# Kernel tuning notes

Measured on AMD Instinct MI355X. Metric: run time of the kernel, lower is better.

The kernel has to match this reference:

```python
import jax, jax.numpy as jnp
import numpy as np

N = 16384
S = 7
B = 2
C = 20
LAMBD_COORD = 5.0
LAMBD_NOOBJ = 0.5
EPS = 1e-6


def _rel2abs(box):
    """Convert (xcr_rcell, ycr_rcell, wr, hr, ...) cell-relative boxes on an
    (N,S,S,>=4) grid to absolute corner boxes (xmin,ymin,xmax,ymax) in [0,1]."""
    col = jnp.arange(S, dtype=box.dtype)[None, None, :]  # x cell index j
    row = jnp.arange(S, dtype=box.dtype)[None, :, None]  # y cell index i
    xc = (box[..., 0] + col) / S
    yc = (box[..., 1] + row) / S
    w = box[..., 2]
    h = box[..., 3]
    half_w = w * 0.5
    half_h = h * 0.5
    return jnp.stack([xc - half_w, yc - half_h, xc + half_w, yc + half_h], axis=-1)


def _iou(b1, b2):
    """Elementwise IoU of corner boxes (..., 4)."""
    xi1 = jnp.maximum(b1[..., 0], b2[..., 0])
    yi1 = jnp.maximum(b1[..., 1], b2[..., 1])
    xi2 = jnp.minimum(b1[..., 2], b2[..., 2])
    yi2 = jnp.minimum(b1[..., 3], b2[..., 3])
    inter = jnp.clip(xi2 - xi1, 0.0) * jnp.clip(yi2 - yi1, 0.0)
    a1 = (b1[..., 2] - b1[..., 0]) * (b1[..., 3] - b1[..., 1])
    a2 = (b2[..., 2] - b2[..., 0]) * (b2[..., 3] - b2[..., 1])
    return inter / (a1 + a2 - inter + EPS)


def setup_inputs() -> dict:
    key = jax.random.key(0)
    k1, k2, k3, k4 = jax.random.split(key, 4)
    prediction = jax.random.uniform(k1, (N, S, S, B * 5 + C), dtype=jnp.float32)
    conf = (jax.random.uniform(k2, (N, S, S)) > 0.7).astype(jnp.float32)[..., None]
    boxes = jax.random.uniform(k3, (N, S, S, 4), dtype=jnp.float32) * conf
    cls = jax.nn.one_hot(jax.random.randint(k4, (N, S, S), 0, C), C, dtype=jnp.float32) * conf
    target = jnp.concatenate([boxes, conf, cls], axis=-1)  # (N,S,S,5+C)
    return {"prediction": prediction, "target": target}


def reference(prediction, target):
    n = prediction.shape[0]

    # Absolute boxes; target box zeroed where no object (mul by confidence).
    tgt_abs = _rel2abs(target[..., :5]) * target[..., 4:5]
    pred_abs1 = _rel2abs(prediction[..., :5])
    pred_abs2 = _rel2abs(prediction[..., 5:10])

    iou1 = _iou(tgt_abs, pred_abs1)  # (N,S,S)
    iou2 = _iou(tgt_abs, pred_abs2)

    # Faithful to torch: idx = (iou1 > iou2)*5, i.e. gather box2 when iou1 > iou2.
    pick_box2 = (iou1 > iou2)[..., None]
    xywhc_hat = jnp.where(pick_box2, prediction[..., 5:10], prediction[..., :5])

    xy_hat = xywhc_hat[..., :2]
    wh_hat = xywhc_hat[..., 2:4]
    c_hat = xywhc_hat[..., 4:5]

    xy = target[..., :2]
    wh = target[..., 2:4]
    conf = target[..., 4:5]
    noobj = conf == 0.0  # identity_obj in torch code

    def sse(t, p):
        return jnp.sum((t - p) ** 2)

    # _coordloss: clamp(min=0), zero where noobj, sum-MSE / N
    loss_xy = sse(xy, jnp.where(noobj, 0.0, jnp.clip(xy_hat, 0.0))) / n
    # _sizeloss: clamp(min=0), zero where noobj, sqrt(sum + eps) / N
    loss_wh = jnp.sqrt(sse(wh, jnp.where(noobj, 0.0, jnp.clip(wh_hat, 0.0))) + EPS) / n
    # _confidenceloss: clamp to [0,1], mask, sum-MSE / N (obj and noobj variants)
    c_hat_clamped = jnp.clip(c_hat, 0.0, 1.0)
    loss_conf_obj = sse(conf, jnp.where(noobj, 0.0, c_hat_clamped)) / n
    loss_conf_noobj = sse(conf, jnp.where(~noobj, 0.0, c_hat_clamped)) / n
    # _classloss: no clamp, zero where noobj
    loss_class = sse(target[..., 5:], jnp.where(noobj, 0.0, prediction[..., 10:])) / n

    loss = (LAMBD_COORD * loss_xy + LAMBD_COORD * loss_wh + loss_conf_obj
            + LAMBD_NOOBJ * loss_conf_noobj + loss_class)
    return (loss_xy, loss_wh, loss_conf_obj, loss_conf_noobj, loss_class, loss)
```

## Files before the change

kernel.cpp:

```cpp
#include <hip/hip_runtime.h>
#include <math.h>

constexpr int TOT    = 16384 * 7 * 7;
constexpr int TILE   = 64;
constexpr int NTILES = TOT / TILE;
constexpr int NBLK   = 1280;
constexpr int NSLOT  = 64;
constexpr int SLOT_STRIDE = 32;
constexpr float INV_N = 1.0f / 16384.0f;
constexpr float INV7  = 1.0f / 7.0f;

constexpr int PRED_TILE_B = TILE * 30 * 4;
constexpr int TGT_TILE_B  = TILE * 25 * 4;
constexpr int BUF_B       = 14336;

__device__ __forceinline__ float fast_rcp(float x) {
    return __builtin_amdgcn_rcpf(x);
}

__device__ __forceinline__ void dma16(const void* g, void* lds) {
    __builtin_amdgcn_global_load_lds(
        (const __attribute__((address_space(1))) void*)g,
        (__attribute__((address_space(3))) void*)lds, 16, 0, 0);
}

__global__ __launch_bounds__(64) void yolo_partial(
    const float* __restrict__ pred, const float* __restrict__ tgt,
    float* __restrict__ acc )
{
    __shared__ float4 smem4[2 * BUF_B / 16];
    char* smem = (char*)smem4;

    const int l   = threadIdx.x;
    const int bid = blockIdx.x;

    float a_xy = 0.0f, a_wh = 0.0f, a_co = 0.0f, a_cn = 0.0f, a_cl = 0.0f;

    const int nt = (NTILES - bid + NBLK - 1) / NBLK;

    auto stage = [&](int tile, int b) {
        const char* gp = (const char*)pred + (long)tile * PRED_TILE_B;
        const char* gt = (const char*)tgt  + (long)tile * TGT_TILE_B;
        char* lb = smem + b * BUF_B;
#pragma unroll
        for (int i = 0; i < 7; ++i)
            dma16(gp + (size_t)(l + i * 64) * 16, lb + i * 1024);
        if (l < 32) dma16(gp + (size_t)(l + 448) * 16, lb + 7168);
#pragma unroll
        for (int i = 0; i < 6; ++i)
            dma16(gt + (size_t)(l + i * 64) * 16, lb + 7680 + i * 1024);
        if (l < 16) dma16(gt + (size_t)(l + 384) * 16, lb + 13824);
    };

    stage(bid, 0);
    int buf = 0;

    for (int k = 0; k < nt; ++k) {
        const int tile = bid + k * NBLK;
        if (k + 1 < nt) {
            stage(bid + (k + 1) * NBLK, buf ^ 1);
            asm volatile("s_waitcnt vmcnt(15)" ::: "memory");
        } else {
            asm volatile("s_waitcnt vmcnt(0)" ::: "memory");
        }
        __builtin_amdgcn_sched_barrier(0);

        const float* pred_s = (const float*)(smem + buf * BUF_B);
        const float* tgt_s  = pred_s + TILE * 30;

        const int   cell = tile * TILE + l;
        const int   col  = cell % 7;
        const int   row  = (cell / 7) % 7;
        const float fcol = (float)col, frow = (float)row;

        float pv[30];
        {
            const float2* p2 = reinterpret_cast<const float2*>(pred_s + l * 30);
#pragma unroll
            for (int i = 0; i < 15; ++i) {
                float2 v = p2[i];
                pv[2 * i] = v.x; pv[2 * i + 1] = v.y;
            }
        }
        float tv[25];
        {
            const float* tp = tgt_s + l * 25;
#pragma unroll
            for (int kk = 0; kk < 25; ++kk) tv[kk] = tp[kk];
        }

        const float conf  = tv[4];
        const bool  noobj = (conf == 0.0f);

        float xc = (tv[0] + fcol) * INV7, yc = (tv[1] + frow) * INV7;
        float hw = tv[2] * 0.5f,          hh = tv[3] * 0.5f;
        float tx1 = (xc - hw) * conf, ty1 = (yc - hh) * conf;
        float tx2 = (xc + hw) * conf, ty2 = (yc + hh) * conf;
        float t_area = (tx2 - tx1) * (ty2 - ty1);

        float xc1 = (pv[0] + fcol) * INV7, yc1 = (pv[1] + frow) * INV7;
        float hw1 = pv[2] * 0.5f,          hh1 = pv[3] * 0.5f;
        float bx1 = xc1 - hw1, by1 = yc1 - hh1, bx2 = xc1 + hw1, by2 = yc1 + hh1;
        float xi1 = fmaxf(tx1, bx1), yi1 = fmaxf(ty1, by1);
        float xi2 = fminf(tx2, bx2), yi2 = fminf(ty2, by2);
        float inter1 = fmaxf(xi2 - xi1, 0.0f) * fmaxf(yi2 - yi1, 0.0f);
        float area1  = (bx2 - bx1) * (by2 - by1);
        float iou1 = inter1 * fast_rcp(t_area + area1 - inter1 + 1e-6f);

        float xc2 = (pv[5] + fcol) * INV7, yc2 = (pv[6] + frow) * INV7;
        float hw2 = pv[7] * 0.5f,          hh2 = pv[8] * 0.5f;
        float cx1 = xc2 - hw2, cy1 = yc2 - hh2, cx2 = xc2 + hw2, cy2 = yc2 + hh2;
        float xj1 = fmaxf(tx1, cx1), yj1 = fmaxf(ty1, cy1);
        float xj2 = fminf(tx2, cx2), yj2 = fminf(ty2, cy2);
        float inter2 = fmaxf(xj2 - xj1, 0.0f) * fmaxf(yj2 - yj1, 0.0f);
        float area2  = (cx2 - cx1) * (cy2 - cy1);
        float iou2 = inter2 * fast_rcp(t_area + area2 - inter2 + 1e-6f);

        const bool pick2 = iou1 > iou2;
        float hx  = pick2 ? pv[5] : pv[0];
        float hy  = pick2 ? pv[6] : pv[1];
        float hwv = pick2 ? pv[7] : pv[2];
        float hhv = pick2 ? pv[8] : pv[3];
        float hc  = pick2 ? pv[9] : pv[4];

        float px = noobj ? 0.0f : fmaxf(hx, 0.0f);
        float py = noobj ? 0.0f : fmaxf(hy, 0.0f);
        float dx = tv[0] - px, dy = tv[1] - py;
        a_xy += dx * dx + dy * dy;
        float pw = noobj ? 0.0f : fmaxf(hwv, 0.0f);
        float ph = noobj ? 0.0f : fmaxf(hhv, 0.0f);
        float dw = tv[2] - pw, dh = tv[3] - ph;
        a_wh += dw * dw + dh * dh;
        float cc = fminf(fmaxf(hc, 0.0f), 1.0f);
        float co = noobj ? 0.0f : cc;
        float cn = noobj ? cc : 0.0f;
        float dco = conf - co, dcn = conf - cn;
        a_co += dco * dco;
        a_cn += dcn * dcn;
        float cl = 0.0f;
#pragma unroll
        for (int kk = 0; kk < 20; ++kk) {
            float pc = noobj ? 0.0f : pv[10 + kk];
            float d  = tv[5 + kk] - pc;
            cl += d * d;
        }
        a_cl += cl;

        buf ^= 1;
    }

#pragma unroll
    for (int off = 32; off > 0; off >>= 1) {
        a_xy += __shfl_down(a_xy, off);
        a_wh += __shfl_down(a_wh, off);
        a_co += __shfl_down(a_co, off);
        a_cn += __shfl_down(a_cn, off);
        a_cl += __shfl_down(a_cl, off);
    }
    if (l == 0) {
        float* slot = acc + (bid & (NSLOT - 1)) * SLOT_STRIDE;
        atomicAdd(&slot[0], a_xy);
        atomicAdd(&slot[1], a_wh);
        atomicAdd(&slot[2], a_co);
        atomicAdd(&slot[3], a_cn);
        atomicAdd(&slot[4], a_cl);
    }
}

__global__ __launch_bounds__(64) void yolo_final(
    const float* __restrict__ acc, float* __restrict__ out)
{
    const int l = threadIdx.x;
    float s0 = acc[l * SLOT_STRIDE + 0];
    float s1 = acc[l * SLOT_STRIDE + 1];
    float s2 = acc[l * SLOT_STRIDE + 2];
    float s3 = acc[l * SLOT_STRIDE + 3];
    float s4 = acc[l * SLOT_STRIDE + 4];
#pragma unroll
    for (int off = 32; off > 0; off >>= 1) {
        s0 += __shfl_down(s0, off);
        s1 += __shfl_down(s1, off);
        s2 += __shfl_down(s2, off);
        s3 += __shfl_down(s3, off);
        s4 += __shfl_down(s4, off);
    }
    if (l == 0) {
        float lxy = s0 * INV_N;
        float lwh = sqrtf(s1 + 1e-6f) * INV_N;
        float lco = s2 * INV_N;
        float lcn = s3 * INV_N;
        float lcl = s4 * INV_N;
        out[0] = lxy;
        out[1] = lwh;
        out[2] = lco;
        out[3] = lcn;
        out[4] = lcl;
        out[5] = 5.0f * lxy + 5.0f * lwh + lco + 0.5f * lcn + lcl;
    }
}

extern "C" void kernel_launch(void* const* d_in, const int* in_sizes, int n_in,
                              void* d_out, int out_size, void* d_ws, size_t ws_size,
                              hipStream_t stream)
{
    const float* pred = (const float*)d_in[0];
    const float* tgt  = (const float*)d_in[1];
    float* out = (float*)d_out;
    float* acc = (float*)d_ws;

    hipMemsetAsync(acc, 0, NSLOT * SLOT_STRIDE * sizeof(float), stream);
    yolo_partial<<<NBLK, 64, 0, stream>>>(pred, tgt, acc);
    yolo_final<<<1, 64, 0, stream>>>(acc, out);
}
```

Measured before the change: 38.18 us.

## Load target tiles via registers and replace atomics with per-block partials

Measured after the change: 34.02 us (median of 2 runs). 1.12x faster.

```diff
diff --git a/kernel.cpp b/kernel.cpp
--- a/kernel.cpp
+++ b/kernel.cpp
@@ -5,8 +5,6 @@
 constexpr int TILE   = 64;
 constexpr int NTILES = TOT / TILE;
 constexpr int NBLK   = 1280;
-constexpr int NSLOT  = 64;
-constexpr int SLOT_STRIDE = 32;
 constexpr float INV_N = 1.0f / 16384.0f;
 constexpr float INV7  = 1.0f / 7.0f;
 
@@ -26,7 +24,7 @@
 
 __global__ __launch_bounds__(64) void yolo_partial(
     const float* __restrict__ pred, const float* __restrict__ tgt,
-    float* __restrict__ acc )
+    float* __restrict__ part )
 {
     __shared__ float4 smem4[2 * BUF_B / 16];
     char* smem = (char*)smem4;
@@ -38,27 +36,47 @@
 
     const int nt = (NTILES - bid + NBLK - 1) / NBLK;
 
-    auto stage = [&](int tile, int b) {
-        const char* gp = (const char*)pred + (long)tile * PRED_TILE_B;
-        const char* gt = (const char*)tgt  + (long)tile * TGT_TILE_B;
-        char* lb = smem + b * BUF_B;
-#pragma unroll
-        for (int i = 0; i < 7; ++i)
-            dma16(gp + (size_t)(l + i * 64) * 16, lb + i * 1024);
-        if (l < 32) dma16(gp + (size_t)(l + 448) * 16, lb + 7168);
-#pragma unroll
-        for (int i = 0; i < 6; ++i)
-            dma16(gt + (size_t)(l + i * 64) * 16, lb + 7680 + i * 1024);
-        if (l < 16) dma16(gt + (size_t)(l + 384) * 16, lb + 13824);
-    };
-
-    stage(bid, 0);
+    float4 tr0, tr1, tr2, tr3, tr4, tr5, tr6;
+
+#define LD_TGT(tile_)                                                       \
+    {                                                                       \
+        const float4* gt4 = reinterpret_cast<const float4*>(               \
+            tgt + (long)(tile_) * (TILE * 25));                             \
+        tr0 = gt4[l];        tr1 = gt4[l + 64];  tr2 = gt4[l + 128];        \
+        tr3 = gt4[l + 192];  tr4 = gt4[l + 256]; tr5 = gt4[l + 320];        \
+        if (l < 16) tr6 = gt4[l + 384];                                     \
+    }
+
+#define DMA_PRED(tile_, b)                                                  \
+    {                                                                       \
+        const char* gp = (const char*)pred + (long)(tile_) * PRED_TILE_B;   \
+        char* lb = smem + (b) * BUF_B;                                      \
+        _Pragma("unroll")                                                   \
+        for (int i = 0; i < 7; ++i)                                         \
+            dma16(gp + (size_t)(l + i * 64) * 16, lb + i * 1024);           \
+        if (l < 32) dma16(gp + (size_t)(l + 448) * 16, lb + 7168);          \
+    }
+
+#define ST_TGT(b)                                                           \
+    {                                                                       \
+        float4* st4 = reinterpret_cast<float4*>(smem + (b) * BUF_B + 7680); \
+        st4[l]       = tr0;  st4[l + 64]  = tr1;  st4[l + 128] = tr2;       \
+        st4[l + 192] = tr3;  st4[l + 256] = tr4;  st4[l + 320] = tr5;       \
+        if (l < 16) st4[l + 384] = tr6;                                     \
+    }
+
+    LD_TGT(bid);
+    DMA_PRED(bid, 0);
+    asm volatile("s_waitcnt vmcnt(8)" ::: "memory");
+    __builtin_amdgcn_sched_barrier(0);
+    ST_TGT(0);
     int buf = 0;
 
     for (int k = 0; k < nt; ++k) {
         const int tile = bid + k * NBLK;
         if (k + 1 < nt) {
-            stage(bid + (k + 1) * NBLK, buf ^ 1);
+            LD_TGT(bid + (k + 1) * NBLK);
+            DMA_PRED(bid + (k + 1) * NBLK, buf ^ 1);
             asm volatile("s_waitcnt vmcnt(15)" ::: "memory");
         } else {
             asm volatile("s_waitcnt vmcnt(0)" ::: "memory");
@@ -137,15 +155,21 @@
         float dco = conf - co, dcn = conf - cn;
         a_co += dco * dco;
         a_cn += dcn * dcn;
-        float cl = 0.0f;
+        float clv = 0.0f;
 #pragma unroll
         for (int kk = 0; kk < 20; ++kk) {
             float pc = noobj ? 0.0f : pv[10 + kk];
             float d  = tv[5 + kk] - pc;
-            cl += d * d;
-        }
-        a_cl += cl;
-
+            clv += d * d;
+        }
+        a_cl += clv;
+
+        if (k + 1 < nt) {
+            asm volatile("s_waitcnt vmcnt(8)" ::: "memory");
+            __builtin_amdgcn_sched_barrier(0);
+            ST_TGT(buf ^ 1);
+            __builtin_amdgcn_sched_barrier(0);
+        }
         buf ^= 1;
     }
 
@@ -158,24 +182,26 @@
         a_cl += __shfl_down(a_cl, off);
     }
     if (l == 0) {
-        float* slot = acc + (bid & (NSLOT - 1)) * SLOT_STRIDE;
-        atomicAdd(&slot[0], a_xy);
-        atomicAdd(&slot[1], a_wh);
-        atomicAdd(&slot[2], a_co);
-        atomicAdd(&slot[3], a_cn);
-        atomicAdd(&slot[4], a_cl);
-    }
-}
-
-__global__ __launch_bounds__(64) void yolo_final(
-    const float* __restrict__ acc, float* __restrict__ out)
+        float4* r = reinterpret_cast<float4*>(part + bid * 8);
+        r[0] = make_float4(a_xy, a_wh, a_co, a_cn);
+        r[1] = make_float4(a_cl, 0.0f, 0.0f, 0.0f);
+    }
+#undef LD_TGT
+#undef DMA_PRED
+#undef ST_TGT
+}
+
+__global__ __launch_bounds__(256) void yolo_final(
+    const float* __restrict__ part, float* __restrict__ out)
 {
-    const int l = threadIdx.x;
-    float s0 = acc[l * SLOT_STRIDE + 0];
-    float s1 = acc[l * SLOT_STRIDE + 1];
-    float s2 = acc[l * SLOT_STRIDE + 2];
-    float s3 = acc[l * SLOT_STRIDE + 3];
-    float s4 = acc[l * SLOT_STRIDE + 4];
+    const int t = threadIdx.x;
+    float s0 = 0.0f, s1 = 0.0f, s2 = 0.0f, s3 = 0.0f, s4 = 0.0f;
+#pragma unroll
+    for (int i = 0; i < NBLK / 256; ++i) {
+        const float4* r = reinterpret_cast<const float4*>(part + (t + i * 256) * 8);
+        float4 v0 = r[0], v1 = r[1];
+        s0 += v0.x; s1 += v0.y; s2 += v0.z; s3 += v0.w; s4 += v1.x;
+    }
 #pragma unroll
     for (int off = 32; off > 0; off >>= 1) {
         s0 += __shfl_down(s0, off);
@@ -184,12 +210,24 @@
         s3 += __shfl_down(s3, off);
         s4 += __shfl_down(s4, off);
     }
-    if (l == 0) {
-        float lxy = s0 * INV_N;
-        float lwh = sqrtf(s1 + 1e-6f) * INV_N;
-        float lco = s2 * INV_N;
-        float lcn = s3 * INV_N;
-        float lcl = s4 * INV_N;
+    __shared__ float red[4][5];
+    const int lane = t & 63, wid = t >> 6;
+    if (lane == 0) {
+        red[wid][0] = s0; red[wid][1] = s1; red[wid][2] = s2;
+        red[wid][3] = s3; red[wid][4] = s4;
+    }
+    __syncthreads();
+    if (t == 0) {
+        float r0 = red[0][0] + red[1][0] + red[2][0] + red[3][0];
+        float r1 = red[0][1] + red[1][1] + red[2][1] + red[3][1];
+        float r2 = red[0][2] + red[1][2] + red[2][2] + red[3][2];
+        float r3 = red[0][3] + red[1][3] + red[2][3] + red[3][3];
+        float r4 = red[0][4] + red[1][4] + red[2][4] + red[3][4];
+        float lxy = r0 * INV_N;
+        float lwh = sqrtf(r1 + 1e-6f) * INV_N;
+        float lco = r2 * INV_N;
+        float lcn = r3 * INV_N;
+        float lcl = r4 * INV_N;
         out[0] = lxy;
         out[1] = lwh;
         out[2] = lco;
@@ -205,10 +243,9 @@
 {
     const float* pred = (const float*)d_in[0];
     const float* tgt  = (const float*)d_in[1];
-    float* out = (float*)d_out;
-    float* acc = (float*)d_ws;
-
-    hipMemsetAsync(acc, 0, NSLOT * SLOT_STRIDE * sizeof(float), stream);
-    yolo_partial<<<NBLK, 64, 0, stream>>>(pred, tgt, acc);
-    yolo_final<<<1, 64, 0, stream>>>(acc, out);
-}
+    float* out  = (float*)d_out;
+    float* part = (float*)d_ws;
+
+    yolo_partial<<<NBLK, 64, 0, stream>>>(pred, tgt, part);
+    yolo_final<<<1, 256, 0, stream>>>(part, out);
+}
```
